# Kernel tuning notes

Hardware: AMD Instinct MI355X
Metric: run time of the kernel (lower is better)

## Reference

```python
import jax, jax.numpy as jnp
import numpy as np

P, L, E, D, NL, FF = 1024, 32, 512, 768, 6, 3072
H_PA, H_TR = 4, 8
VOCAB = 256


def layer_norm(x, w, b, eps=1e-5):
    mu = x.mean(-1, keepdims=True)
    var = ((x - mu) ** 2).mean(-1, keepdims=True)
    return (x - mu) / jnp.sqrt(var + eps) * w + b


def mha(x, wqkv, bqkv, wo, bo, nheads, key_mask=None):
    # x: [B,S,E]; torch nn.MultiheadAttention semantics (scale q by 1/sqrt(d))
    B, S, Emb = x.shape
    d = Emb // nheads
    qkv = x @ wqkv.T + bqkv
    q, k, v = jnp.split(qkv, 3, axis=-1)
    hd = lambda t: t.reshape(B, S, nheads, d).transpose(0, 2, 1, 3)
    q, k, v = hd(q) * (d ** -0.5), hd(k), hd(v)
    scores = jnp.einsum('bhqd,bhkd->bhqk', q, k)
    if key_mask is not None:
        scores = jnp.where(key_mask[:, None, None, :], scores, -1e9)
    a = jax.nn.softmax(scores, axis=-1)
    o = jnp.einsum('bhqk,bhkd->bhqd', a, v).transpose(0, 2, 1, 3).reshape(B, S, Emb)
    return o @ wo.T + bo


def setup_inputs() -> dict:
    key = jax.random.key(0)
    ks = jax.random.split(key, 32)
    n = lambda i, shape, s=0.02: (jax.random.normal(ks[i], shape, dtype=jnp.float32) * s)
    x = lambda i, shape: jax.random.normal(ks[i], shape, dtype=jnp.float32) * (1.0 / np.sqrt(shape[-1]))
    tokens = jax.random.randint(ks[0], (P, L), 0, VOCAB, dtype=jnp.int32)
    lengths = jax.random.randint(ks[1], (P,), 4, L + 1, dtype=jnp.int32)
    byte_emb = n(2, (VOCAB, E)).at[0].set(0.0)  # padding_idx=0
    inp = {
        'tokens': tokens, 'lengths': lengths,
        'byte_emb': byte_emb,
        'local_pos_emb': n(3, (L, E)),
        'patch_pos_emb': n(4, (P, D)),
        'pa_qkv_w': x(5, (3 * E, E)), 'pa_qkv_b': jnp.zeros((3 * E,), jnp.float32),
        'pa_out_w': x(6, (E, E)), 'pa_out_b': jnp.zeros((E,), jnp.float32),
        'proj_w': x(7, (D, E)), 'proj_b': jnp.zeros((D,), jnp.float32),
        'layers_qkv_w': x(8, (NL, 3 * D, D)), 'layers_qkv_b': jnp.zeros((NL, 3 * D), jnp.float32),
        'layers_out_w': x(9, (NL, D, D)), 'layers_out_b': jnp.zeros((NL, D), jnp.float32),
        'layers_ln1_w': jnp.ones((NL, D), jnp.float32), 'layers_ln1_b': jnp.zeros((NL, D), jnp.float32),
        'layers_ln2_w': jnp.ones((NL, D), jnp.float32), 'layers_ln2_b': jnp.zeros((NL, D), jnp.float32),
        'layers_ff1_w': x(10, (NL, FF, D)), 'layers_ff1_b': jnp.zeros((NL, FF), jnp.float32),
        'layers_ff2_w': x(11, (NL, D, FF)), 'layers_ff2_b': jnp.zeros((NL, D), jnp.float32),
        'ln_f_w': jnp.ones((D,), jnp.float32), 'ln_f_b': jnp.zeros((D,), jnp.float32),
    }
    return inp


def reference(tokens, lengths, byte_emb, local_pos_emb, patch_pos_emb,
              pa_qkv_w, pa_qkv_b, pa_out_w, pa_out_b, proj_w, proj_b,
              layers_qkv_w, layers_qkv_b, layers_out_w, layers_out_b,
              layers_ln1_w, layers_ln1_b, layers_ln2_w, layers_ln2_b,
              layers_ff1_w, layers_ff1_b, layers_ff2_w, layers_ff2_b,
              ln_f_w, ln_f_b):
    mask = jnp.arange(L) < lengths[:, None]  # [P,L] valid-byte mask
    # encode_patches: byte embed + local positions, zero padded slots
    emb = byte_emb[tokens] + local_pos_emb[None, :, :]  # [P,L,E]
    emb = emb * mask[..., None].astype(emb.dtype)
    # per-patch MHA over bytes (key padding mask), vectorized across patches
    attn = mha(emb, pa_qkv_w, pa_qkv_b, pa_out_w, pa_out_b, H_PA, key_mask=mask)
    cnt = mask.sum(-1, keepdims=True).astype(emb.dtype)
    patch_repr = (attn * mask[..., None].astype(emb.dtype)).sum(1) / cnt  # [P,E] masked mean
    # project to hidden and add patch-level positions
    h = patch_repr @ proj_w.T + proj_b + patch_pos_emb[:P]
    h = h[None]  # [1,P,D]
    # pre-norm transformer encoder, gelu FFN
    for i in range(NL):
        hn = layer_norm(h, layers_ln1_w[i], layers_ln1_b[i])
        h = h + mha(hn, layers_qkv_w[i], layers_qkv_b[i], layers_out_w[i], layers_out_b[i], H_TR)
        hn = layer_norm(h, layers_ln2_w[i], layers_ln2_b[i])
        ff = jax.nn.gelu(hn @ layers_ff1_w[i].T + layers_ff1_b[i], approximate=False)
        h = h + ff @ layers_ff2_w[i].T + layers_ff2_b[i]
    return layer_norm(h, ln_f_w, ln_f_b)[0]  # [P,D]
```

## Files before the change

### kernel.cpp

```cpp
#include <hip/hip_runtime.h>
#include <hip/hip_bf16.h>
#include <math.h>

typedef __hip_bfloat16 bf16;
typedef unsigned short u16;
typedef __attribute__((ext_vector_type(8))) short short8;
typedef __attribute__((ext_vector_type(4))) float f32x4;

#define PP 1024
#define LL 32
#define EE 512
#define DD 768
#define NLAYER 6
#define FFDIM 3072

__device__ __forceinline__ float bf2f(u16 u) { return __uint_as_float(((unsigned)u) << 16); }
__device__ __forceinline__ u16 f2b(float x) {
  unsigned u = __float_as_uint(x);
  return (u16)((u + 0x7FFFu + ((u >> 16) & 1u)) >> 16);
}

__global__ __launch_bounds__(256) void cvt4(
    const float* s0, const float* s1, const float* s2, const float* s3,
    u16* d0, u16* d1, u16* d2, u16* d3,
    int n0, int n1, int n2, int n3)
{
  int r = blockIdx.y;
  const float* s = r == 0 ? s0 : r == 1 ? s1 : r == 2 ? s2 : s3;
  u16* d        = r == 0 ? d0 : r == 1 ? d1 : r == 2 ? d2 : d3;
  int n4        = r == 0 ? n0 : r == 1 ? n1 : r == 2 ? n2 : n3;
  int i = blockIdx.x * 256 + threadIdx.x;
  if (i < n4) {
    float4 v = ((const float4*)s)[i];
    ushort4 o;
    o.x = f2b(v.x); o.y = f2b(v.y); o.z = f2b(v.z); o.w = f2b(v.w);
    ((ushort4*)d)[i] = o;
  }
}

__global__ __launch_bounds__(256) void embed_table(
    const float* __restrict__ be, const float* __restrict__ lp, bf16* __restrict__ T)
{
  int i = blockIdx.x * 256 + threadIdx.x;
  int r = i >> 6, c = (i & 63) << 3;
  int t = r >> 5, l = r & 31;
  const float* bp = be + ((long)t << 9) + c;
  const float* pp = lp + ((long)l << 9) + c;
  float4 x0 = *(const float4*)bp, x1 = *(const float4*)(bp + 4);
  float4 y0 = *(const float4*)pp, y1 = *(const float4*)(pp + 4);
  short8 o;
  o[0] = (short)f2b(x0.x + y0.x); o[1] = (short)f2b(x0.y + y0.y);
  o[2] = (short)f2b(x0.z + y0.z); o[3] = (short)f2b(x0.w + y0.w);
  o[4] = (short)f2b(x1.x + y1.x); o[5] = (short)f2b(x1.y + y1.y);
  o[6] = (short)f2b(x1.z + y1.z); o[7] = (short)f2b(x1.w + y1.w);
  *(short8*)((u16*)T + ((long)r << 9) + c) = o;
}

__global__ __launch_bounds__(256) void gemm64(
    const bf16* A, long sAb, int lda,
    const bf16* B, long sBb, int ldb,
    float* Cf, bf16* Cb, long sCb, int ldc,
    const float* bias, int biasStride,
    const float* addf,
    int M, int N, int K, int act)
{
  __shared__ u16 As[2][64][72];
  __shared__ u16 Bs[2][64][72];
  const int bz = blockIdx.z;
  const u16* Ap = (const u16*)A + (long)bz * sAb;
  const u16* Bp = (const u16*)B + (long)bz * sBb;
  const long coff = (long)bz * sCb;
  const int m0 = blockIdx.x << 6, n0 = blockIdx.y << 6;
  const int tid = threadIdx.x;
  const int wave = tid >> 6, lane = tid & 63;
  const int sr = tid >> 3;
  const int scc = (tid & 7) << 3;
  const int br0 = n0 + sr, br1 = n0 + sr + 32;
  const short8 zz = {0,0,0,0,0,0,0,0};
  f32x4 acc[4] = {{0.f,0.f,0.f,0.f},{0.f,0.f,0.f,0.f},{0.f,0.f,0.f,0.f},{0.f,0.f,0.f,0.f}};

  {
    int ch = K < 64 ? K : 64;
    bool kv = scc < ch;
    short8 a0 = zz, a1 = zz, b0 = zz, b1 = zz;
    if (kv) {
      a0 = *(const short8*)(Ap + (long)(m0 + sr) * lda + scc);
      a1 = *(const short8*)(Ap + (long)(m0 + sr + 32) * lda + scc);
      if (br0 < N) b0 = *(const short8*)(Bp + (long)br0 * ldb + scc);
      if (br1 < N) b1 = *(const short8*)(Bp + (long)br1 * ldb + scc);
    }
    *(short8*)&As[0][sr][scc] = a0;
    *(short8*)&As[0][sr + 32][scc] = a1;
    *(short8*)&Bs[0][sr][scc] = b0;
    *(short8*)&Bs[0][sr + 32][scc] = b1;
  }
  __syncthreads();

  const int arow = (wave << 4) + (lane & 15);
  const int kq = (lane >> 4) << 3;
  int buf = 0;
  for (int k0 = 0; k0 < K; k0 += 64) {
    int knext = k0 + 64;
    bool more = knext < K;
    short8 a0 = zz, a1 = zz, b0 = zz, b1 = zz;
    if (more) {
      int ch = K - knext; if (ch > 64) ch = 64;
      bool kv = scc < ch;
      if (kv) {
        a0 = *(const short8*)(Ap + (long)(m0 + sr) * lda + knext + scc);
        a1 = *(const short8*)(Ap + (long)(m0 + sr + 32) * lda + knext + scc);
        if (br0 < N) b0 = *(const short8*)(Bp + (long)br0 * ldb + knext + scc);
        if (br1 < N) b1 = *(const short8*)(Bp + (long)br1 * ldb + knext + scc);
      }
    }
    int rem = K - k0; if (rem > 64) rem = 64;
    {
      short8 af = *(const short8*)&As[buf][arow][kq];
#pragma unroll
      for (int nt = 0; nt < 4; nt++) {
        short8 bfr = *(const short8*)&Bs[buf][(nt << 4) + (lane & 15)][kq];
        acc[nt] = __builtin_amdgcn_mfma_f32_16x16x32_bf16(af, bfr, acc[nt], 0, 0, 0);
      }
    }
    if (rem > 32) {
      short8 af = *(const short8*)&As[buf][arow][32 + kq];
#pragma unroll
      for (int nt = 0; nt < 4; nt++) {
        short8 bfr = *(const short8*)&Bs[buf][(nt << 4) + (lane & 15)][32 + kq];
        acc[nt] = __builtin_amdgcn_mfma_f32_16x16x32_bf16(af, bfr, acc[nt], 0, 0, 0);
      }
    }
    if (more) {
      int nb = buf ^ 1;
      *(short8*)&As[nb][sr][scc] = a0;
      *(short8*)&As[nb][sr + 32][scc] = a1;
      *(short8*)&Bs[nb][sr][scc] = b0;
      *(short8*)&Bs[nb][sr + 32][scc] = b1;
      __syncthreads();
      buf = nb;
    }
  }

  int rbase = m0 + (wave << 4) + ((lane >> 4) << 2);
#pragma unroll
  for (int nt = 0; nt < 4; nt++) {
    int c = n0 + (nt << 4) + (lane & 15);
    if (c >= N) continue;
    float bvl = bias ? bias[bz * biasStride + c] : 0.f;
    if (act == 2 && bz != 0) bvl = 0.f;
#pragma unroll
    for (int j = 0; j < 4; j++) {
      int r = rbase + j;
      long idx = coff + (long)r * ldc + c;
      float v = acc[nt][j] + bvl;
      if (addf) v += addf[idx];
      if (act == 1) v = 0.5f * v * (1.f + erff(v * 0.70710678118654752f));
      if (Cf) Cf[idx] = v;
      if (Cb) Cb[idx] = __float2bfloat16(v);
    }
  }
}

__global__ __launch_bounds__(256) void patch_attn(
    const bf16* __restrict__ qkt,
    const int* __restrict__ tokens, const int* __restrict__ lengths,
    const float* __restrict__ byte_emb, const float* __restrict__ local_pos,
    bf16* __restrict__ Z)
{
  __shared__ float wsum[4][32];
  __shared__ int tok_s[32];
  __shared__ int cnt_s;
  int p = blockIdx.x;
  int tid = threadIdx.x;
  if (tid < 32) tok_s[tid] = tokens[p * 32 + tid];
  if (tid == 0) cnt_s = lengths[p];
  __syncthreads();
  int cnt = cnt_s;
  int h = tid >> 6, lane = tid & 63;
  const int rsel = lane & 15;
  const int ksel = (lane >> 4) << 3;
  const u16* qkb = (const u16*)qkt + h * 128;
  const long r0 = ((long)((tok_s[rsel] << 5) | rsel)) << 10;
  const long r1 = ((long)((tok_s[16 + rsel] << 5) | (16 + rsel))) << 10;

  f32x4 acc[2][2] = {{{0.f,0.f,0.f,0.f},{0.f,0.f,0.f,0.f}},
                     {{0.f,0.f,0.f,0.f},{0.f,0.f,0.f,0.f}}};
#pragma unroll
  for (int kc = 0; kc < 4; kc++) {
    int ko = kc * 32 + ksel;
    short8 a0 = *(const short8*)(qkb + r0 + ko);
    short8 a1 = *(const short8*)(qkb + r1 + ko);
    short8 b0 = *(const short8*)(qkb + r0 + 512 + ko);
    short8 b1 = *(const short8*)(qkb + r1 + 512 + ko);
    acc[0][0] = __builtin_amdgcn_mfma_f32_16x16x32_bf16(a0, b0, acc[0][0], 0, 0, 0);
    acc[0][1] = __builtin_amdgcn_mfma_f32_16x16x32_bf16(a0, b1, acc[0][1], 0, 0, 0);
    acc[1][0] = __builtin_amdgcn_mfma_f32_16x16x32_bf16(a1, b0, acc[1][0], 0, 0, 0);
    acc[1][1] = __builtin_amdgcn_mfma_f32_16x16x32_bf16(a1, b1, acc[1][1], 0, 0, 0);
  }

  const float scale = 0.088388347648318447f;
  int j0 = lane & 15, j1 = 16 + j0;
  bool v0 = j0 < cnt, v1 = j1 < cnt;
  int rowq = (lane >> 4) << 2;
  float cs0 = 0.f, cs1 = 0.f;
#pragma unroll
  for (int ti = 0; ti < 2; ti++) {
    float s0[4], s1[4], mx[4], sm[4], e0[4], e1[4];
#pragma unroll
    for (int r = 0; r < 4; r++) {
      s0[r] = acc[ti][0][r] * scale;
      s1[r] = acc[ti][1][r] * scale;
      float a = v0 ? s0[r] : -1e30f;
      float b = v1 ? s1[r] : -1e30f;
      mx[r] = fmaxf(a, b);
    }
#pragma unroll
    for (int d = 1; d < 16; d <<= 1)
#pragma unroll
      for (int r = 0; r < 4; r++) mx[r] = fmaxf(mx[r], __shfl_xor(mx[r], d));
#pragma unroll
    for (int r = 0; r < 4; r++) {
      e0[r] = v0 ? __expf(s0[r] - mx[r]) : 0.f;
      e1[r] = v1 ? __expf(s1[r] - mx[r]) : 0.f;
      sm[r] = e0[r] + e1[r];
    }
#pragma unroll
    for (int d = 1; d < 16; d <<= 1)
#pragma unroll
      for (int r = 0; r < 4; r++) sm[r] += __shfl_xor(sm[r], d);
#pragma unroll
    for (int r = 0; r < 4; r++) {
      int row = ti * 16 + rowq + r;
      if (row < cnt) {
        float inv = 1.f / sm[r];
        cs0 += e0[r] * inv;
        cs1 += e1[r] * inv;
      }
    }
  }
  cs0 += __shfl_xor(cs0, 16); cs0 += __shfl_xor(cs0, 32);
  cs1 += __shfl_xor(cs1, 16); cs1 += __shfl_xor(cs1, 32);
  if (lane < 16) {
    float invc = 1.f / (float)cnt;
    wsum[h][lane] = cs0 * invc;
    wsum[h][16 + lane] = cs1 * invc;
  }
  __syncthreads();

  for (int e = tid; e < 512; e += 256) {
    float za0 = 0.f, za1 = 0.f, za2 = 0.f, za3 = 0.f;
    for (int j = 0; j < cnt; j++) {
      float ev = byte_emb[((long)tok_s[j] << 9) + e] + local_pos[((long)j << 9) + e];
      za0 += wsum[0][j] * ev;
      za1 += wsum[1][j] * ev;
      za2 += wsum[2][j] * ev;
      za3 += wsum[3][j] * ev;
    }
    long zb = (long)p * 2048;
    Z[zb + e]        = __float2bfloat16(za0);
    Z[zb + 512 + e]  = __float2bfloat16(za1);
    Z[zb + 1024 + e] = __float2bfloat16(za2);
    Z[zb + 1536 + e] = __float2bfloat16(za3);
  }
}

__global__ __launch_bounds__(256) void ln_kernel(
    const float* __restrict__ x,
    const float* __restrict__ a0, const float* __restrict__ a1,
    const float* __restrict__ a2, const float* __restrict__ a3,
    float* __restrict__ hout,
    const float* __restrict__ w, const float* __restrict__ b,
    bf16* outb, float* outf)
{
  __shared__ float red[8];
  __shared__ float mv[2];
  int row = blockIdx.x;
  long base = (long)row * DD;
  int tid = threadIdx.x, lane = tid & 63, wave = tid >> 6;
  float vv[3];
  float s = 0.f, s2 = 0.f;
#pragma unroll
  for (int j = 0; j < 3; j++) {
    long c = base + tid + j * 256;
    float v = x[c];
    if (a0) v += a0[c];
    if (a1) v += a1[c];
    if (a2) v += a2[c];
    if (a3) v += a3[c];
    if (hout) hout[c] = v;
    vv[j] = v; s += v; s2 += v * v;
  }
  for (int o = 32; o; o >>= 1) { s += __shfl_down(s, o); s2 += __shfl_down(s2, o); }
  if (lane == 0) { red[wave] = s; red[4 + wave] = s2; }
  __syncthreads();
  if (tid == 0) {
    float ts = red[0] + red[1] + red[2] + red[3];
    float ts2 = red[4] + red[5] + red[6] + red[7];
    float mu = ts / DD;
    float var = ts2 / DD - mu * mu;
    mv[0] = mu; mv[1] = rsqrtf(var + 1e-5f);
  }
  __syncthreads();
  float mu = mv[0], rstd = mv[1];
#pragma unroll
  for (int j = 0; j < 3; j++) {
    int c = tid + j * 256;
    float v = (vv[j] - mu) * rstd * w[c] + b[c];
    if (outb) outb[base + c] = __float2bfloat16(v);
    if (outf) outf[base + c] = v;
  }
}

__global__ __launch_bounds__(256) void softmax_bf(u16* __restrict__ S)
{
  __shared__ float red[4], red2[4];
  long row = blockIdx.x;
  u16* sr = S + row * 1024;
  int tid = threadIdx.x, lane = tid & 63, wave = tid >> 6;
  const float scale = 0.10206207261596577f;
  ushort4 raw = *(const ushort4*)(sr + tid * 4);
  float v[4] = {bf2f(raw.x) * scale, bf2f(raw.y) * scale, bf2f(raw.z) * scale, bf2f(raw.w) * scale};
  float m = fmaxf(fmaxf(v[0], v[1]), fmaxf(v[2], v[3]));
  for (int o = 32; o; o >>= 1) m = fmaxf(m, __shfl_down(m, o));
  if (lane == 0) red[wave] = m;
  __syncthreads();
  m = fmaxf(fmaxf(red[0], red[1]), fmaxf(red[2], red[3]));
  float s = 0.f;
#pragma unroll
  for (int k = 0; k < 4; k++) { v[k] = __expf(v[k] - m); s += v[k]; }
  for (int o = 32; o; o >>= 1) s += __shfl_down(s, o);
  if (lane == 0) red2[wave] = s;
  __syncthreads();
  s = red2[0] + red2[1] + red2[2] + red2[3];
  float inv = 1.f / s;
  ushort4 o4;
  o4.x = f2b(v[0] * inv); o4.y = f2b(v[1] * inv); o4.z = f2b(v[2] * inv); o4.w = f2b(v[3] * inv);
  *(ushort4*)(sr + tid * 4) = o4;
}

__global__ __launch_bounds__(256) void transpose_v(
    const bf16* __restrict__ qkv, bf16* __restrict__ Vt)
{
  __shared__ u16 tile[32][33];
  int k0 = blockIdx.x << 5;
  int d0 = blockIdx.y << 5;
  int tx = threadIdx.x & 31, ty = threadIdx.x >> 5;
  const u16* q = (const u16*)qkv;
  for (int i = ty; i < 32; i += 8)
    tile[i][tx] = q[(long)(k0 + i) * 2304 + 1536 + d0 + tx];
  __syncthreads();
  u16* vt = (u16*)Vt;
  for (int i = ty; i < 32; i += 8)
    vt[(long)(d0 + i) * 1024 + k0 + tx] = tile[tx][i];
}

extern "C" void kernel_launch(void* const* d_in, const int* in_sizes, int n_in,
                              void* d_out, int out_size, void* d_ws, size_t ws_size,
                              hipStream_t stream)
{
  const int*   tokens    = (const int*)d_in[0];
  const int*   lengths   = (const int*)d_in[1];
  const float* byte_emb  = (const float*)d_in[2];
  const float* local_pos = (const float*)d_in[3];
  const float* patch_pos = (const float*)d_in[4];
  const float* pa_qkv_w  = (const float*)d_in[5];
  const float* pa_qkv_b  = (const float*)d_in[6];
  const float* pa_out_w  = (const float*)d_in[7];
  const float* pa_out_b  = (const float*)d_in[8];
  const float* proj_w    = (const float*)d_in[9];
  const float* proj_b    = (const float*)d_in[10];
  const float* Wqkv      = (const float*)d_in[11];
  const float* Bqkv      = (const float*)d_in[12];
  const float* Wout      = (const float*)d_in[13];
  const float* Bout      = (const float*)d_in[14];
  const float* ln1w      = (const float*)d_in[15];
  const float* ln1b      = (const float*)d_in[16];
  const float* ln2w      = (const float*)d_in[17];
  const float* ln2b      = (const float*)d_in[18];
  const float* W1        = (const float*)d_in[19];
  const float* B1        = (const float*)d_in[20];
  const float* W2        = (const float*)d_in[21];
  const float* B2        = (const float*)d_in[22];
  const float* lnfw      = (const float*)d_in[23];
  const float* lnfb      = (const float*)d_in[24];

  char* ws = (char*)d_ws;
  const size_t MB = 1ull << 20;
  bf16* qkT    = (bf16*)(ws);
  u16*  scores = (u16*)(ws);
  bf16* qkvt   = (bf16*)(ws + 16 * MB);
  bf16* Vt     = (bf16*)(ws + 21 * MB);
  bf16* attn   = (bf16*)(ws + 23 * MB);
  bf16* ffb    = (bf16*)(ws + 25 * MB);
  float* h     = (float*)(ws + 31 * MB);
  bf16* hn     = (bf16*)(ws + 34 * MB);
  u16*  Lw     = (u16*)(ws + 36 * MB);
  bf16* embT   = (bf16*)(ws + 50 * MB);
  float* hp    = (float*)(ws + 58 * MB);
  bf16* Z      = (bf16*)(ws + 64 * MB);
  bf16* o_mean = (bf16*)(ws + 68 * MB);
  bf16* t1     = (bf16*)(ws + 69 * MB);
  u16*  P1w    = (u16*)(ws + 70 * MB);

  const long PSTRIDE = (long)PP * DD;

  const long oLQKV = 0;
  const long oLOUT = 1769472;
  const long oLW1  = 2359296;
  const long oLW2  = 4718592;
  const long oPAQ  = 0;
  const long oPAO  = 786432;
  const long oPRJ  = 1048576;

  cvt4<<<dim3(768, 3), 256, 0, stream>>>(
      pa_qkv_w, pa_out_w, proj_w, nullptr,
      P1w + oPAQ, P1w + oPAO, P1w + oPRJ, nullptr,
      786432 / 4, 262144 / 4, 393216 / 4, 0);
  embed_table<<<2048, 256, 0, stream>>>(byte_emb, local_pos, embT);
  gemm64<<<dim3(128, 16, 1), 256, 0, stream>>>(
      embT, 0, EE, (bf16*)(P1w + oPAQ), 0, EE, nullptr, qkT, 0, 1024,
      pa_qkv_b, 0, nullptr, 8192, 1024, EE, 0);
  patch_attn<<<PP, 256, 0, stream>>>(
      qkT, tokens, lengths, byte_emb, local_pos, Z);
  gemm64<<<dim3(16, 2, 4), 256, 0, stream>>>(
      Z, 512, 2048, (bf16*)(P1w + oPAQ + 1024L * EE), 128L * EE, EE,
      nullptr, o_mean, 128, EE, pa_qkv_b + 1024, 128, nullptr, PP, 128, EE, 0);
  gemm64<<<dim3(16, 8, 1), 256, 0, stream>>>(
      o_mean, 0, EE, (bf16*)(P1w + oPAO), 0, EE, nullptr, t1, 0, EE,
      pa_out_b, 0, nullptr, PP, EE, EE, 0);
  gemm64<<<dim3(16, 12, 1), 256, 0, stream>>>(
      t1, 0, EE, (bf16*)(P1w + oPRJ), 0, EE, h, nullptr, 0, DD,
      proj_b, 0, patch_pos, PP, DD, EE, 0);

  for (int i = 0; i < NLAYER; i++) {
    cvt4<<<dim3(2304, 4), 256, 0, stream>>>(
        Wqkv + (long)i * 2304 * DD, Wout + (long)i * DD * DD,
        W1 + (long)i * FFDIM * DD, W2 + (long)i * DD * FFDIM,
        Lw + oLQKV, Lw + oLOUT, Lw + oLW1, Lw + oLW2,
        1769472 / 4, 589824 / 4, 2359296 / 4, 2359296 / 4);
    if (i == 0)
      ln_kernel<<<PP, 256, 0, stream>>>(h, nullptr, nullptr, nullptr, nullptr,
                                        nullptr, ln1w + i * DD, ln1b + i * DD, hn, nullptr);
    else
      ln_kernel<<<PP, 256, 0, stream>>>(h, hp, hp + PSTRIDE, hp + 2 * PSTRIDE, hp + 3 * PSTRIDE,
                                        h, ln1w + i * DD, ln1b + i * DD, hn, nullptr);
    gemm64<<<dim3(16, 36, 1), 256, 0, stream>>>(
        hn, 0, DD, (bf16*)(Lw + oLQKV), 0, DD, nullptr, qkvt, 0, 2304,
        Bqkv + i * 2304, 0, nullptr, PP, 2304, DD, 0);
    gemm64<<<dim3(16, 16, 8), 256, 0, stream>>>(
        qkvt, 96, 2304, qkvt + DD, 96, 2304, nullptr, (bf16*)scores, 1024L * 1024, 1024,
        nullptr, 0, nullptr, 1024, 1024, 96, 0);
    softmax_bf<<<8192, 256, 0, stream>>>(scores);
    transpose_v<<<dim3(32, 24), 256, 0, stream>>>(qkvt, Vt);
    gemm64<<<dim3(16, 2, 8), 256, 0, stream>>>(
        (bf16*)scores, 1024L * 1024, 1024, Vt, 96L * 1024, 1024, nullptr, attn, 96, DD,
        nullptr, 0, nullptr, 1024, 96, 1024, 0);
    gemm64<<<dim3(16, 12, 2), 256, 0, stream>>>(
        attn, 384, DD, (bf16*)(Lw + oLOUT), 384, DD, hp, nullptr, PSTRIDE, DD,
        Bout + i * DD, 0, nullptr, PP, DD, 384, 2);
    ln_kernel<<<PP, 256, 0, stream>>>(h, hp, hp + PSTRIDE, nullptr, nullptr,
                                      h, ln2w + i * DD, ln2b + i * DD, hn, nullptr);
    gemm64<<<dim3(16, 48, 1), 256, 0, stream>>>(
        hn, 0, DD, (bf16*)(Lw + oLW1), 0, DD, nullptr, ffb, 0, FFDIM,
        B1 + i * FFDIM, 0, nullptr, PP, FFDIM, DD, 1);
    gemm64<<<dim3(16, 12, 4), 256, 0, stream>>>(
        ffb, 768, FFDIM, (bf16*)(Lw + oLW2), 768, FFDIM, hp, nullptr, PSTRIDE, DD,
        B2 + i * DD, 0, nullptr, PP, DD, 768, 2);
  }
  ln_kernel<<<PP, 256, 0, stream>>>(h, hp, hp + PSTRIDE, hp + 2 * PSTRIDE, hp + 3 * PSTRIDE,
                                    nullptr, lnfw, lnfb, nullptr, (float*)d_out);
}
```

Measured before the change: 988.6 us.

## Fuse transformer self-attention into flash-style MFMA kernel with online softmax

Replaces the three-kernel attention path (QK^T GEMM writing a bf16 score matrix, a separate softmax pass, then a PV GEMM) with one kernel that computes scores per 32-key tile in registers, keeps a running max and sum, and accumulates P·V with MFMA. This removes the 8x1024x1024 score matrix round trip through memory and two launches per layer. The cost is a small grid (256 blocks of 2 waves) with no LDS staging of K/V, so each wave reloads K and V from global memory or cache, and occupancy on a large GPU may be low.

New measurement: 1.010 ms. 1.02x slower.

```diff
diff --git a/kernel.cpp b/kernel.cpp
--- a/kernel.cpp
+++ b/kernel.cpp
@@ -6,6 +6,7 @@
 typedef unsigned short u16;
 typedef __attribute__((ext_vector_type(8))) short short8;
 typedef __attribute__((ext_vector_type(4))) float f32x4;
+typedef __attribute__((ext_vector_type(4))) unsigned u32x4;
 
 #define PP 1024
 #define LL 32
@@ -161,6 +162,116 @@
   }
 }
 
+__global__ __launch_bounds__(128) void fused_attn(
+    const bf16* __restrict__ qkvt,
+    const bf16* __restrict__ Vt,
+    bf16* __restrict__ attn)
+{
+  const int h = blockIdx.y;
+  const int wid = threadIdx.x >> 6;
+  const int lane = threadIdx.x & 63;
+  const int q0 = (blockIdx.x << 5) + (wid << 4);
+  const int lr = lane & 15;
+  const int lq = lane >> 4;
+  const float scale = 0.10206207261596577f;
+
+  const u16* qp = (const u16*)qkvt;
+  const u16* kp = qp + 768 + h * 96 + (lq << 3);
+  const u16* vp = (const u16*)Vt + ((long)(h * 96 + lr) << 10) + (lq << 3);
+
+  short8 qf[3];
+#pragma unroll
+  for (int c = 0; c < 3; c++)
+    qf[c] = *(const short8*)(qp + (long)(q0 + lr) * 2304 + h * 96 + (c << 5) + (lq << 3));
+
+  f32x4 o[6] = {{0.f,0.f,0.f,0.f},{0.f,0.f,0.f,0.f},{0.f,0.f,0.f,0.f},
+                {0.f,0.f,0.f,0.f},{0.f,0.f,0.f,0.f},{0.f,0.f,0.f,0.f}};
+  float m = -INFINITY, l = 0.f;
+
+  for (int k0 = 0; k0 < 1024; k0 += 32) {
+    f32x4 s0 = {0.f,0.f,0.f,0.f}, s1 = {0.f,0.f,0.f,0.f};
+#pragma unroll
+    for (int c = 0; c < 3; c++) {
+      short8 kf0 = *(const short8*)(kp + (long)(k0 + lr) * 2304 + (c << 5));
+      short8 kf1 = *(const short8*)(kp + (long)(k0 + 16 + lr) * 2304 + (c << 5));
+      s0 = __builtin_amdgcn_mfma_f32_16x16x32_bf16(kf0, qf[c], s0, 0, 0, 0);
+      s1 = __builtin_amdgcn_mfma_f32_16x16x32_bf16(kf1, qf[c], s1, 0, 0, 0);
+    }
+    float e0[4], e1[4];
+    float mx = -INFINITY;
+#pragma unroll
+    for (int r = 0; r < 4; r++) {
+      e0[r] = s0[r] * scale;
+      e1[r] = s1[r] * scale;
+      mx = fmaxf(mx, fmaxf(e0[r], e1[r]));
+    }
+    mx = fmaxf(mx, __shfl_xor(mx, 16));
+    mx = fmaxf(mx, __shfl_xor(mx, 32));
+    float mn = fmaxf(m, mx);
+    float ts = 0.f;
+#pragma unroll
+    for (int r = 0; r < 4; r++) {
+      e0[r] = __expf(e0[r] - mn);
+      e1[r] = __expf(e1[r] - mn);
+      ts += e0[r] + e1[r];
+    }
+    ts += __shfl_xor(ts, 16);
+    ts += __shfl_xor(ts, 32);
+    if (!__all(mx <= m)) {
+      float f = __expf(m - mn);
+      float fr[4];
+#pragma unroll
+      for (int r = 0; r < 4; r++) fr[r] = __shfl(f, (lq << 2) + r);
+#pragma unroll
+      for (int n = 0; n < 6; n++)
+#pragma unroll
+        for (int r = 0; r < 4; r++) o[n][r] *= fr[r];
+      l *= f;
+    }
+    l += ts;
+    m = mn;
+
+    unsigned a01 = ((unsigned)f2b(e0[1]) << 16) | f2b(e0[0]);
+    unsigned a23 = ((unsigned)f2b(e0[3]) << 16) | f2b(e0[2]);
+    unsigned b01 = ((unsigned)f2b(e1[1]) << 16) | f2b(e1[0]);
+    unsigned b23 = ((unsigned)f2b(e1[3]) << 16) | f2b(e1[2]);
+    int sA = lr + ((lq & 1) << 5);
+    int sB = sA + 16;
+    unsigned qa01 = (unsigned)__shfl((int)a01, sA);
+    unsigned qa23 = (unsigned)__shfl((int)a23, sA);
+    unsigned qb01 = (unsigned)__shfl((int)b01, sA);
+    unsigned qb23 = (unsigned)__shfl((int)b23, sA);
+    unsigned ra01 = (unsigned)__shfl((int)a01, sB);
+    unsigned ra23 = (unsigned)__shfl((int)a23, sB);
+    unsigned rb01 = (unsigned)__shfl((int)b01, sB);
+    unsigned rb23 = (unsigned)__shfl((int)b23, sB);
+    bool hi = lq >= 2;
+    u32x4 wv;
+    wv[0] = hi ? qb01 : qa01;
+    wv[1] = hi ? qb23 : qa23;
+    wv[2] = hi ? rb01 : ra01;
+    wv[3] = hi ? rb23 : ra23;
+    short8 pa = __builtin_bit_cast(short8, wv);
+
+#pragma unroll
+    for (int n = 0; n < 6; n++) {
+      short8 vf = *(const short8*)(vp + (long)(n << 4) * 1024 + k0);
+      o[n] = __builtin_amdgcn_mfma_f32_16x16x32_bf16(pa, vf, o[n], 0, 0, 0);
+    }
+  }
+
+  float inv = 1.f / l;
+  float ir[4];
+#pragma unroll
+  for (int r = 0; r < 4; r++) ir[r] = __shfl(inv, (lq << 2) + r);
+  u16* op = (u16*)attn + (long)(q0 + (lq << 2)) * 768 + h * 96 + lr;
+#pragma unroll
+  for (int r = 0; r < 4; r++)
+#pragma unroll
+    for (int n = 0; n < 6; n++)
+      op[(long)r * 768 + (n << 4)] = f2b(o[n][r] * ir[r]);
+}
+
 __global__ __launch_bounds__(256) void patch_attn(
     const bf16* __restrict__ qkt,
     const int* __restrict__ tokens, const int* __restrict__ lengths,
@@ -309,33 +420,6 @@
     if (outb) outb[base + c] = __float2bfloat16(v);
     if (outf) outf[base + c] = v;
   }
-}
-
-__global__ __launch_bounds__(256) void softmax_bf(u16* __restrict__ S)
-{
-  __shared__ float red[4], red2[4];
-  long row = blockIdx.x;
-  u16* sr = S + row * 1024;
-  int tid = threadIdx.x, lane = tid & 63, wave = tid >> 6;
-  const float scale = 0.10206207261596577f;
-  ushort4 raw = *(const ushort4*)(sr + tid * 4);
-  float v[4] = {bf2f(raw.x) * scale, bf2f(raw.y) * scale, bf2f(raw.z) * scale, bf2f(raw.w) * scale};
-  float m = fmaxf(fmaxf(v[0], v[1]), fmaxf(v[2], v[3]));
-  for (int o = 32; o; o >>= 1) m = fmaxf(m, __shfl_down(m, o));
-  if (lane == 0) red[wave] = m;
-  __syncthreads();
-  m = fmaxf(fmaxf(red[0], red[1]), fmaxf(red[2], red[3]));
-  float s = 0.f;
-#pragma unroll
-  for (int k = 0; k < 4; k++) { v[k] = __expf(v[k] - m); s += v[k]; }
-  for (int o = 32; o; o >>= 1) s += __shfl_down(s, o);
-  if (lane == 0) red2[wave] = s;
-  __syncthreads();
-  s = red2[0] + red2[1] + red2[2] + red2[3];
-  float inv = 1.f / s;
-  ushort4 o4;
-  o4.x = f2b(v[0] * inv); o4.y = f2b(v[1] * inv); o4.z = f2b(v[2] * inv); o4.w = f2b(v[3] * inv);
-  *(ushort4*)(sr + tid * 4) = o4;
 }
 
 __global__ __launch_bounds__(256) void transpose_v(
@@ -387,7 +471,6 @@
   char* ws = (char*)d_ws;
   const size_t MB = 1ull << 20;
   bf16* qkT    = (bf16*)(ws);
-  u16*  scores = (u16*)(ws);
   bf16* qkvt   = (bf16*)(ws + 16 * MB);
   bf16* Vt     = (bf16*)(ws + 21 * MB);
   bf16* attn   = (bf16*)(ws + 23 * MB);
@@ -447,14 +530,8 @@
     gemm64<<<dim3(16, 36, 1), 256, 0, stream>>>(
         hn, 0, DD, (bf16*)(Lw + oLQKV), 0, DD, nullptr, qkvt, 0, 2304,
         Bqkv + i * 2304, 0, nullptr, PP, 2304, DD, 0);
-    gemm64<<<dim3(16, 16, 8), 256, 0, stream>>>(
-        qkvt, 96, 2304, qkvt + DD, 96, 2304, nullptr, (bf16*)scores, 1024L * 1024, 1024,
-        nullptr, 0, nullptr, 1024, 1024, 96, 0);
-    softmax_bf<<<8192, 256, 0, stream>>>(scores);
     transpose_v<<<dim3(32, 24), 256, 0, stream>>>(qkvt, Vt);
-    gemm64<<<dim3(16, 2, 8), 256, 0, stream>>>(
-        (bf16*)scores, 1024L * 1024, 1024, Vt, 96L * 1024, 1024, nullptr, attn, 96, DD,
-        nullptr, 0, nullptr, 1024, 96, 1024, 0);
+    fused_attn<<<dim3(32, 8), 128, 0, stream>>>(qkvt, Vt, attn);
     gemm64<<<dim3(16, 12, 2), 256, 0, stream>>>(
         attn, 384, DD, (bf16*)(Lw + oLOUT), 384, DD, hp, nullptr, PSTRIDE, DD,
         Bout + i * DD, 0, nullptr, PP, DD, 384, 2);
```
